# Optimization experiments

Hardware: AMD Instinct MI355X
Metric: run time of the kernel (lower is better)

Reference implementation:

```python
import jax, jax.numpy as jnp
import numpy as np

T = 128        # number of time points
D = 64         # flattened state dim (bs * z_dim, bs = 1)
H = 256        # hidden width of f-network
HK = 128       # hidden width of kernel network
MAX_IT = 3     # fixed-point iterations (args.max_iterations)


def setup_inputs() -> dict:
    key = jax.random.key(0)
    ks = jax.random.split(key, 6)
    g = lambda k, sh, sc: (jax.random.normal(k, sh, jnp.float32) * sc)
    z0 = jax.random.normal(ks[0], (1, D), jnp.float32)
    t = jnp.linspace(0.0, 1.0, T, dtype=jnp.float32)
    # f: D -> H -> D MLP (the 'func' integrand network)
    W1 = g(ks[1], (D, H), 1.0 / np.sqrt(D)); b1 = jnp.zeros((H,), jnp.float32)
    W2 = g(ks[2], (H, D), 1.0 / np.sqrt(H)); b2 = jnp.zeros((D,), jnp.float32)
    # kernel: (x, s) -> D*D matrix entries (the neural kernel K)
    Wk1 = g(ks[3], (2, HK), 1.0 / np.sqrt(2.0)); bk1 = jnp.zeros((HK,), jnp.float32)
    Wk2 = g(ks[4], (HK, D * D), 1.0 / np.sqrt(HK)); bk2 = jnp.zeros((D * D,), jnp.float32)
    return dict(z0=z0, t=t, W1=W1, b1=b1, W2=W2, b2=b2,
                Wk1=Wk1, bk1=bk1, Wk2=Wk2, bk2=bk2)


def _trapezoid_weights(t):
    """w[i, j]: trapezoid quadrature weight of node j for integral over [t0, t_i]."""
    dt = t[1] - t[0]  # uniform grid
    idx = jnp.arange(T)
    mask = (idx[None, :] <= idx[:, None]).astype(t.dtype)
    w = dt * mask
    w = w.at[(idx, idx)].multiply(0.5)   # halve right endpoint of each row
    w = w.at[:, 0].multiply(0.5)         # halve left endpoint
    w = w.at[0].set(0.0)                 # zero-length integral at t0
    return w


def _solve(z0, t, W1, b1, W2, b2, Wk1, bk1, Wk2, bk2):
    y0 = z0.reshape(-1)                                   # [D], solver flattens batch
    w = _trapezoid_weights(t)                             # [T, T]
    # Neural kernel K(x_i, s_j) -> [D, D], precomputed once on the grid.
    pairs = jnp.stack([jnp.broadcast_to(t[:, None], (T, T)),
                       jnp.broadcast_to(t[None, :], (T, T))], axis=-1)  # [T, T, 2]
    hK = jnp.tanh(pairs @ Wk1 + bk1)                      # [T, T, HK]
    K = (hK @ Wk2 + bk2).reshape(T, T, D, D)              # [T, T, D, D]

    def f(y):  # integrand network, applied over all time points
        return jnp.tanh(y @ W1 + b1) @ W2 + b2            # [T, D]

    def step(y, _):
        # G_i = \int_0^{x_i} K(x_i, s) f(y(s)) ds  (trapezoid on grid)
        G = jnp.einsum('ij,ijde,je->id', w, K, f(y))      # [T, D]
        # y'(x) = G(x)  =>  y_i = y0 + \int_0^{x_i} G(s) ds
        y_new = y0[None, :] + w @ G                       # [T, D]
        return y_new, None

    y_init = jnp.tile(y0[None, :], (T, 1))                # fixed-point initial guess
    y, _ = jax.lax.scan(step, y_init, None, length=MAX_IT)
    return y


def reference(z0, t, W1, b1, W2, b2, Wk1, bk1, Wk2, bk2):
    y = _solve(z0, t, W1, b1, W2, b2, Wk1, bk1, Wk2, bk2)  # [T, D]
    return y[-1].reshape(1, D)  # z[-1]: final state, shape [bs, dim]
```

## Files before the change

kernel.cpp:

```cpp
#include <hip/hip_runtime.h>
#include <hip/hip_bf16.h>

#define TT 128
#define DD 64
#define HH 256
#define HK 128
#define JH (TT*HK)
#define HD (HK*DD)
#define NCHUNK 64

__global__ void __launch_bounds__(256)
k_F(const float* __restrict__ G, const float* __restrict__ z0,
    const float* __restrict__ t,
    const float* __restrict__ W1, const float* __restrict__ b1,
    const float* __restrict__ W2, const float* __restrict__ b2,
    const float* __restrict__ bk2,
    float* __restrict__ F, float* __restrict__ bF, int it) {
    int j = blockIdx.x, tid = threadIdx.x;
    int part = tid >> 6, d = tid & 63;
    __shared__ float red[4][64];
    __shared__ float ys[DD];
    __shared__ float hs[HH];
    __shared__ float fs[DD];
    float dt = t[1] - t[0];
    if (it == 0) {
        if (tid < DD) ys[tid] = z0[tid];
    } else {
        float s = 0.f;
        if (j > 0) {
            for (int jp = part; jp <= j; jp += 4) {
                float w = (jp == 0 || jp == j) ? 0.5f : 1.0f;
                s += w * G[jp * DD + d];
            }
        }
        red[part][d] = s;
        __syncthreads();
        if (part == 0)
            ys[d] = z0[d] + dt * (red[0][d] + red[1][d] + red[2][d] + red[3][d]);
    }
    __syncthreads();
    float acc = b1[tid];
    #pragma unroll 8
    for (int e = 0; e < DD; ++e) acc += ys[e] * W1[e * HH + tid];
    hs[tid] = tanhf(acc);
    __syncthreads();
    {
        float s = 0.f;
        #pragma unroll 8
        for (int h = part * 64; h < part * 64 + 64; ++h) s += hs[h] * W2[h * DD + d];
        red[part][d] = s;
    }
    __syncthreads();
    if (part == 0) {
        float a = b2[d] + red[0][d] + red[1][d] + red[2][d] + red[3][d];
        fs[d] = a;
        F[j * DD + d] = a;
    }
    __syncthreads();
    {
        float s = 0.f;
        #pragma unroll
        for (int e = part * 16; e < part * 16 + 16; ++e) s += bk2[d * DD + e] * fs[e];
        red[part][d] = s;
    }
    __syncthreads();
    if (part == 0)
        bF[j * DD + d] = red[0][d] + red[1][d] + red[2][d] + red[3][d];
}

__global__ void __launch_bounds__(256)
k_M(const float* __restrict__ F, const float* __restrict__ Wk2,
    float* __restrict__ M) {
    int tid = threadIdx.x;
    int hd = blockIdx.x * 256 + tid;
    int j0 = blockIdx.y * 8;
    __shared__ __attribute__((aligned(16))) float Fs[8][64];
    for (int k = tid; k < 8 * DD; k += 256) Fs[k >> 6][k & 63] = F[j0 * DD + k];
    __syncthreads();
    float acc[8] = {0.f,0.f,0.f,0.f,0.f,0.f,0.f,0.f};
    const float* Wrow = Wk2 + (size_t)(hd >> 6) * (DD * DD) + (size_t)(hd & 63) * DD;
    for (int e = 0; e < DD; e += 8) {
        float4 wa = *(const float4*)(Wrow + e);
        float4 wb = *(const float4*)(Wrow + e + 4);
        #pragma unroll
        for (int r = 0; r < 8; ++r) {
            float4 f0 = *(const float4*)&Fs[r][e];
            float4 f1 = *(const float4*)&Fs[r][e + 4];
            acc[r] += f0.x*wa.x + f0.y*wa.y + f0.z*wa.z + f0.w*wa.w
                    + f1.x*wb.x + f1.y*wb.y + f1.z*wb.z + f1.w*wb.w;
        }
    }
    #pragma unroll
    for (int r = 0; r < 8; ++r) M[(size_t)(j0 + r) * HD + hd] = acc[r];
}

__global__ void __launch_bounds__(256)
k_G1(const float* __restrict__ t, const float* __restrict__ Wk1,
     const float* __restrict__ bk1, const float* __restrict__ M,
     float* __restrict__ P, const float* __restrict__ z0,
     float* __restrict__ out, int final_it) {
    int itile = blockIdx.x, c = blockIdx.y;
    if (c > 4 * itile + 3) return;
    __shared__ __attribute__((aligned(16))) float As[8 * 256];
    __shared__ float red[4][8][64];
    int tid = threadIdx.x, sub = tid >> 6, d = tid & 63;

    {
        float dt = t[1] - t[0];
        int h = tid & 127;
        int j = 2 * c + (tid >> 7);
        float wk0 = Wk1[h], wk1v = Wk1[HK + h], bk = bk1[h];
        float tj = t[j];
        #pragma unroll
        for (int k = 0; k < 8; ++k) {
            int i = itile * 8 + k;
            float w = (i == 0 || j > i) ? 0.f : dt * ((j == 0 || j == i) ? 0.5f : 1.0f);
            As[k * 256 + tid] = w * tanhf(t[i] * wk0 + tj * wk1v + bk);
        }
    }
    if (final_it && itile == 0 && c == 0 && tid < DD) out[tid] = z0[tid];
    __syncthreads();

    float acc[8] = {0.f,0.f,0.f,0.f,0.f,0.f,0.f,0.f};
    const float* Mp = M + ((size_t)c * 256) * DD + d;
    int jl0 = sub * 64;
    for (int jl = jl0; jl < jl0 + 64; jl += 8) {
        float m0 = Mp[(size_t)(jl + 0) * DD];
        float m1 = Mp[(size_t)(jl + 1) * DD];
        float m2 = Mp[(size_t)(jl + 2) * DD];
        float m3 = Mp[(size_t)(jl + 3) * DD];
        float m4 = Mp[(size_t)(jl + 4) * DD];
        float m5 = Mp[(size_t)(jl + 5) * DD];
        float m6 = Mp[(size_t)(jl + 6) * DD];
        float m7 = Mp[(size_t)(jl + 7) * DD];
        #pragma unroll
        for (int r = 0; r < 8; ++r) {
            float4 a0 = *(const float4*)&As[r * 256 + jl];
            float4 a1 = *(const float4*)&As[r * 256 + jl + 4];
            acc[r] += a0.x*m0 + a0.y*m1 + a0.z*m2 + a0.w*m3
                    + a1.x*m4 + a1.y*m5 + a1.z*m6 + a1.w*m7;
        }
    }
    #pragma unroll
    for (int r = 0; r < 8; ++r) red[sub][r][d] = acc[r];
    __syncthreads();
    if (sub == 0) {
        #pragma unroll
        for (int r = 0; r < 8; ++r) {
            float v = red[0][r][d] + red[1][r][d] + red[2][r][d] + red[3][r][d];
            P[(size_t)c * (TT * DD) + (itile * 8 + r) * DD + d] = v;
        }
    }
}

__global__ void __launch_bounds__(256)
k_Gfin(const float* __restrict__ P, const float* __restrict__ bF,
       const float* __restrict__ t, float* __restrict__ G,
       float* __restrict__ out, int final_it) {
    int j = blockIdx.x, tid = threadIdx.x;
    int part = tid >> 6, d = tid & 63;
    __shared__ float red[4][64];
    float dt = t[1] - t[0];
    float a = 0.f;
    int cmax = j >> 1;
    for (int c = part; c <= cmax; c += 4) a += P[(size_t)c * (TT * DD) + j * DD + d];
    if (j > 0) {
        float s = 0.f;
        for (int jp = part; jp <= j; jp += 4) {
            float w = (jp == 0 || jp == j) ? 0.5f : 1.0f;
            s += w * bF[jp * DD + d];
        }
        a += dt * s;
    }
    red[part][d] = a;
    __syncthreads();
    if (part == 0) {
        float v = red[0][d] + red[1][d] + red[2][d] + red[3][d];
        G[j * DD + d] = v;
        if (final_it) {
            float wj = (j == 0 || j == TT - 1) ? 0.5f : 1.0f;
            atomicAdd(&out[d], dt * wj * v);
        }
    }
}

extern "C" void kernel_launch(void* const* d_in, const int* in_sizes, int n_in,
                              void* d_out, int out_size, void* d_ws, size_t ws_size,
                              hipStream_t stream) {
    const float* z0  = (const float*)d_in[0];
    const float* t   = (const float*)d_in[1];
    const float* W1  = (const float*)d_in[2];
    const float* b1  = (const float*)d_in[3];
    const float* W2  = (const float*)d_in[4];
    const float* b2  = (const float*)d_in[5];
    const float* Wk1 = (const float*)d_in[6];
    const float* bk1 = (const float*)d_in[7];
    const float* Wk2 = (const float*)d_in[8];
    const float* bk2 = (const float*)d_in[9];
    float* out = (float*)d_out;

    float* ws = (float*)d_ws;
    float* M  = ws;
    float* F  = M  + (size_t)TT*HK*DD;
    float* bF = F  + TT*DD;
    float* G  = bF + TT*DD;
    float* P  = G  + TT*DD;

    for (int it = 0; it < 3; ++it) {
        int fin = (it == 2) ? 1 : 0;
        k_F<<<TT, 256, 0, stream>>>(G, z0, t, W1, b1, W2, b2, bk2, F, bF, it);
        k_M<<<dim3(32, 16), 256, 0, stream>>>(F, Wk2, M);
        k_G1<<<dim3(16, NCHUNK), 256, 0, stream>>>(t, Wk1, bk1, M, P, z0, out, fin);
        k_Gfin<<<TT, 256, 0, stream>>>(P, bF, t, G, out, fin);
    }
}
```

Measured before the change: 201.5 us.

## Fuse G finalization into next F kernel and widen G1 chunks

Removes the per-iteration G-finalization kernel by folding the reduction of partial sums and the bias-kernel term directly into the next iteration's F computation, which now builds y from P and the previous bF via a prefix-sum loop. The G1 kernel now uses 1024-wide j chunks (16 chunks instead of 64), so fewer partial-sum slices need reducing, at the cost of more work per block and fewer blocks. Ping-pong bF buffers are introduced and the launch sequence is unrolled. The F kernel now does serial per-row prefix work and loads up to 128x64 bF into shared memory, which adds latency per block.

```diff
diff --git a/kernel.cpp b/kernel.cpp
--- a/kernel.cpp
+++ b/kernel.cpp
@@ -7,37 +7,22 @@
 #define HK 128
 #define JH (TT*HK)
 #define HD (HK*DD)
-#define NCHUNK 64
-
-__global__ void __launch_bounds__(256)
-k_F(const float* __restrict__ G, const float* __restrict__ z0,
-    const float* __restrict__ t,
-    const float* __restrict__ W1, const float* __restrict__ b1,
-    const float* __restrict__ W2, const float* __restrict__ b2,
-    const float* __restrict__ bk2,
-    float* __restrict__ F, float* __restrict__ bF, int it) {
+#define NCHUNK 16
+#define CW 1024
+
+__global__ void __launch_bounds__(256)
+k_F0(const float* __restrict__ z0,
+     const float* __restrict__ W1, const float* __restrict__ b1,
+     const float* __restrict__ W2, const float* __restrict__ b2,
+     const float* __restrict__ bk2,
+     float* __restrict__ F, float* __restrict__ bF) {
     int j = blockIdx.x, tid = threadIdx.x;
     int part = tid >> 6, d = tid & 63;
     __shared__ float red[4][64];
     __shared__ float ys[DD];
     __shared__ float hs[HH];
     __shared__ float fs[DD];
-    float dt = t[1] - t[0];
-    if (it == 0) {
-        if (tid < DD) ys[tid] = z0[tid];
-    } else {
-        float s = 0.f;
-        if (j > 0) {
-            for (int jp = part; jp <= j; jp += 4) {
-                float w = (jp == 0 || jp == j) ? 0.5f : 1.0f;
-                s += w * G[jp * DD + d];
-            }
-        }
-        red[part][d] = s;
-        __syncthreads();
-        if (part == 0)
-            ys[d] = z0[d] + dt * (red[0][d] + red[1][d] + red[2][d] + red[3][d]);
-    }
+    if (tid < DD) ys[tid] = z0[tid];
     __syncthreads();
     float acc = b1[tid];
     #pragma unroll 8
@@ -66,6 +51,95 @@
     __syncthreads();
     if (part == 0)
         bF[j * DD + d] = red[0][d] + red[1][d] + red[2][d] + red[3][d];
+}
+
+__global__ void __launch_bounds__(256)
+k_FP(const float* __restrict__ P, const float* __restrict__ bFin,
+     const float* __restrict__ z0, const float* __restrict__ t,
+     const float* __restrict__ W1, const float* __restrict__ b1,
+     const float* __restrict__ W2, const float* __restrict__ b2,
+     const float* __restrict__ bk2,
+     float* __restrict__ F, float* __restrict__ bFout) {
+    int j = blockIdx.x, tid = threadIdx.x;
+    int part = tid >> 6, d = tid & 63;
+    __shared__ float bfs[TT][DD];
+    __shared__ float red[4][64];
+    __shared__ float ys[DD];
+    __shared__ float hs[HH];
+    __shared__ float fs[DD];
+    float dt = t[1] - t[0];
+
+    for (int k = tid; k < (j + 1) * DD; k += 256) bfs[k >> 6][k & 63] = bFin[k];
+
+    float s1 = 0.f;
+    for (int p = part; p <= j; p += 4) {
+        if (p == 0) continue;
+        int cmax = p >> 3;
+        float a = 0.f;
+        int c = 0;
+        for (; c + 7 <= cmax; c += 8) {
+            float p0 = P[(size_t)(c + 0) * (TT * DD) + p * DD + d];
+            float p1 = P[(size_t)(c + 1) * (TT * DD) + p * DD + d];
+            float p2 = P[(size_t)(c + 2) * (TT * DD) + p * DD + d];
+            float p3 = P[(size_t)(c + 3) * (TT * DD) + p * DD + d];
+            float p4 = P[(size_t)(c + 4) * (TT * DD) + p * DD + d];
+            float p5 = P[(size_t)(c + 5) * (TT * DD) + p * DD + d];
+            float p6 = P[(size_t)(c + 6) * (TT * DD) + p * DD + d];
+            float p7 = P[(size_t)(c + 7) * (TT * DD) + p * DD + d];
+            a += ((p0 + p1) + (p2 + p3)) + ((p4 + p5) + (p6 + p7));
+        }
+        for (; c <= cmax; ++c) a += P[(size_t)c * (TT * DD) + p * DD + d];
+        float wp = (p == j) ? 0.5f : 1.0f;
+        s1 += wp * a;
+    }
+    red[part][d] = s1;
+    __syncthreads();
+
+    if (part == 0) {
+        float sT = 0.f;
+        if (j > 0) {
+            float B0 = bfs[0][d];
+            float S = B0;
+            for (int p = 1; p <= j; ++p) {
+                float Bp = bfs[p][d];
+                float bft = dt * (S - 0.5f * B0 + 0.5f * Bp);
+                float wp = (p == j) ? 0.5f : 1.0f;
+                sT += wp * bft;
+                S += Bp;
+            }
+        }
+        float Bsum = red[0][d] + red[1][d] + red[2][d] + red[3][d];
+        ys[d] = z0[d] + dt * (Bsum + sT);
+    }
+    __syncthreads();
+
+    float acc = b1[tid];
+    #pragma unroll 8
+    for (int e = 0; e < DD; ++e) acc += ys[e] * W1[e * HH + tid];
+    hs[tid] = tanhf(acc);
+    __syncthreads();
+    {
+        float s = 0.f;
+        #pragma unroll 8
+        for (int h = part * 64; h < part * 64 + 64; ++h) s += hs[h] * W2[h * DD + d];
+        red[part][d] = s;
+    }
+    __syncthreads();
+    if (part == 0) {
+        float a = b2[d] + red[0][d] + red[1][d] + red[2][d] + red[3][d];
+        fs[d] = a;
+        F[j * DD + d] = a;
+    }
+    __syncthreads();
+    {
+        float s = 0.f;
+        #pragma unroll
+        for (int e = part * 16; e < part * 16 + 16; ++e) s += bk2[d * DD + e] * fs[e];
+        red[part][d] = s;
+    }
+    __syncthreads();
+    if (part == 0)
+        bFout[j * DD + d] = red[0][d] + red[1][d] + red[2][d] + red[3][d];
 }
 
 __global__ void __launch_bounds__(256)
@@ -100,31 +174,38 @@
      float* __restrict__ P, const float* __restrict__ z0,
      float* __restrict__ out, int final_it) {
     int itile = blockIdx.x, c = blockIdx.y;
-    if (c > 4 * itile + 3) return;
-    __shared__ __attribute__((aligned(16))) float As[8 * 256];
+    if (c > itile) return;
+    __shared__ __attribute__((aligned(16))) float As[8 * CW];
     __shared__ float red[4][8][64];
     int tid = threadIdx.x, sub = tid >> 6, d = tid & 63;
 
     {
         float dt = t[1] - t[0];
-        int h = tid & 127;
-        int j = 2 * c + (tid >> 7);
+        int h = tid & 127, jhi = tid >> 7;
         float wk0 = Wk1[h], wk1v = Wk1[HK + h], bk = bk1[h];
-        float tj = t[j];
-        #pragma unroll
-        for (int k = 0; k < 8; ++k) {
-            int i = itile * 8 + k;
-            float w = (i == 0 || j > i) ? 0.f : dt * ((j == 0 || j == i) ? 0.5f : 1.0f);
-            As[k * 256 + tid] = w * tanhf(t[i] * wk0 + tj * wk1v + bk);
+        float ti[8];
+        #pragma unroll
+        for (int k = 0; k < 8; ++k) ti[k] = t[itile * 8 + k];
+        #pragma unroll
+        for (int jj = 0; jj < 4; ++jj) {
+            int jloc = jj * 2 + jhi;
+            int j = c * 8 + jloc;
+            float tj = t[j];
+            #pragma unroll
+            for (int k = 0; k < 8; ++k) {
+                int i = itile * 8 + k;
+                float w = (i == 0 || j > i) ? 0.f : dt * ((j == 0 || j == i) ? 0.5f : 1.0f);
+                As[k * CW + jloc * HK + h] = w * tanhf(ti[k] * wk0 + tj * wk1v + bk);
+            }
         }
     }
     if (final_it && itile == 0 && c == 0 && tid < DD) out[tid] = z0[tid];
     __syncthreads();
 
     float acc[8] = {0.f,0.f,0.f,0.f,0.f,0.f,0.f,0.f};
-    const float* Mp = M + ((size_t)c * 256) * DD + d;
-    int jl0 = sub * 64;
-    for (int jl = jl0; jl < jl0 + 64; jl += 8) {
+    const float* Mp = M + ((size_t)c * CW) * DD + d;
+    int jl0 = sub * 256;
+    for (int jl = jl0; jl < jl0 + 256; jl += 8) {
         float m0 = Mp[(size_t)(jl + 0) * DD];
         float m1 = Mp[(size_t)(jl + 1) * DD];
         float m2 = Mp[(size_t)(jl + 2) * DD];
@@ -135,8 +216,8 @@
         float m7 = Mp[(size_t)(jl + 7) * DD];
         #pragma unroll
         for (int r = 0; r < 8; ++r) {
-            float4 a0 = *(const float4*)&As[r * 256 + jl];
-            float4 a1 = *(const float4*)&As[r * 256 + jl + 4];
+            float4 a0 = *(const float4*)&As[r * CW + jl];
+            float4 a1 = *(const float4*)&As[r * CW + jl + 4];
             acc[r] += a0.x*m0 + a0.y*m1 + a0.z*m2 + a0.w*m3
                     + a1.x*m4 + a1.y*m5 + a1.z*m6 + a1.w*m7;
         }
@@ -154,15 +235,14 @@
 }
 
 __global__ void __launch_bounds__(256)
-k_Gfin(const float* __restrict__ P, const float* __restrict__ bF,
-       const float* __restrict__ t, float* __restrict__ G,
-       float* __restrict__ out, int final_it) {
+k_out2(const float* __restrict__ P, const float* __restrict__ bF,
+       const float* __restrict__ t, float* __restrict__ out) {
     int j = blockIdx.x, tid = threadIdx.x;
     int part = tid >> 6, d = tid & 63;
     __shared__ float red[4][64];
     float dt = t[1] - t[0];
     float a = 0.f;
-    int cmax = j >> 1;
+    int cmax = j >> 3;
     for (int c = part; c <= cmax; c += 4) a += P[(size_t)c * (TT * DD) + j * DD + d];
     if (j > 0) {
         float s = 0.f;
@@ -176,11 +256,8 @@
     __syncthreads();
     if (part == 0) {
         float v = red[0][d] + red[1][d] + red[2][d] + red[3][d];
-        G[j * DD + d] = v;
-        if (final_it) {
-            float wj = (j == 0 || j == TT - 1) ? 0.5f : 1.0f;
-            atomicAdd(&out[d], dt * wj * v);
-        }
+        float wj = (j == 0 || j == TT - 1) ? 0.5f : 1.0f;
+        atomicAdd(&out[d], dt * wj * v);
     }
 }
 
@@ -199,18 +276,21 @@
     const float* bk2 = (const float*)d_in[9];
     float* out = (float*)d_out;
 
-    float* ws = (float*)d_ws;
-    float* M  = ws;
-    float* F  = M  + (size_t)TT*HK*DD;
-    float* bF = F  + TT*DD;
-    float* G  = bF + TT*DD;
-    float* P  = G  + TT*DD;
-
-    for (int it = 0; it < 3; ++it) {
-        int fin = (it == 2) ? 1 : 0;
-        k_F<<<TT, 256, 0, stream>>>(G, z0, t, W1, b1, W2, b2, bk2, F, bF, it);
-        k_M<<<dim3(32, 16), 256, 0, stream>>>(F, Wk2, M);
-        k_G1<<<dim3(16, NCHUNK), 256, 0, stream>>>(t, Wk1, bk1, M, P, z0, out, fin);
-        k_Gfin<<<TT, 256, 0, stream>>>(P, bF, t, G, out, fin);
-    }
-}
+    float* ws  = (float*)d_ws;
+    float* M   = ws;
+    float* F   = M   + (size_t)TT*HK*DD;
+    float* bFA = F   + TT*DD;
+    float* bFB = bFA + TT*DD;
+    float* P   = bFB + TT*DD;
+
+    k_F0<<<TT, 256, 0, stream>>>(z0, W1, b1, W2, b2, bk2, F, bFA);
+    k_M<<<dim3(32, 16), 256, 0, stream>>>(F, Wk2, M);
+    k_G1<<<dim3(16, NCHUNK), 256, 0, stream>>>(t, Wk1, bk1, M, P, z0, out, 0);
+    k_FP<<<TT, 256, 0, stream>>>(P, bFA, z0, t, W1, b1, W2, b2, bk2, F, bFB);
+    k_M<<<dim3(32, 16), 256, 0, stream>>>(F, Wk2, M);
+    k_G1<<<dim3(16, NCHUNK), 256, 0, stream>>>(t, Wk1, bk1, M, P, z0, out, 0);
+    k_FP<<<TT, 256, 0, stream>>>(P, bFB, z0, t, W1, b1, W2, b2, bk2, F, bFA);
+    k_M<<<dim3(32, 16), 256, 0, stream>>>(F, Wk2, M);
+    k_G1<<<dim3(16, NCHUNK), 256, 0, stream>>>(t, Wk1, bk1, M, P, z0, out, 1);
+    k_out2<<<TT, 256, 0, stream>>>(P, bFA, t, out);
+}
```

After: 260.3 us. 29.2% more time.

## Fuse M projection into the f-network kernel, dropping the F buffer

Applied to the files above, without the earlier changes.

Merges k_M into k_F so that each time-point block computes its own row of M = F·Wk2 right after evaluating f, which removes one launch per iteration and the F round trip through global memory. The trade-off is reuse: each block now streams all of Wk2 (2 MB) for a single f row, where the old k_M amortized every Wk2 load over 8 rows. Only 128 blocks run the heavy part, so L2 traffic on Wk2 rises about eightfold and parallelism drops.

```diff
diff --git a/kernel.cpp b/kernel.cpp
--- a/kernel.cpp
+++ b/kernel.cpp
@@ -10,12 +10,12 @@
 #define NCHUNK 64
 
 __global__ void __launch_bounds__(256)
-k_F(const float* __restrict__ G, const float* __restrict__ z0,
-    const float* __restrict__ t,
-    const float* __restrict__ W1, const float* __restrict__ b1,
-    const float* __restrict__ W2, const float* __restrict__ b2,
-    const float* __restrict__ bk2,
-    float* __restrict__ F, float* __restrict__ bF, int it) {
+k_FM2(const float* __restrict__ G, const float* __restrict__ z0,
+      const float* __restrict__ t,
+      const float* __restrict__ W1, const float* __restrict__ b1,
+      const float* __restrict__ W2, const float* __restrict__ b2,
+      const float* __restrict__ bk2, const float* __restrict__ Wk2,
+      float* __restrict__ M, float* __restrict__ bF, int it) {
     int j = blockIdx.x, tid = threadIdx.x;
     int part = tid >> 6, d = tid & 63;
     __shared__ float red[4][64];
@@ -23,6 +23,7 @@
     __shared__ float hs[HH];
     __shared__ float fs[DD];
     float dt = t[1] - t[0];
+
     if (it == 0) {
         if (tid < DD) ys[tid] = z0[tid];
     } else {
@@ -39,6 +40,7 @@
             ys[d] = z0[d] + dt * (red[0][d] + red[1][d] + red[2][d] + red[3][d]);
     }
     __syncthreads();
+
     float acc = b1[tid];
     #pragma unroll 8
     for (int e = 0; e < DD; ++e) acc += ys[e] * W1[e * HH + tid];
@@ -51,12 +53,10 @@
         red[part][d] = s;
     }
     __syncthreads();
-    if (part == 0) {
-        float a = b2[d] + red[0][d] + red[1][d] + red[2][d] + red[3][d];
-        fs[d] = a;
-        F[j * DD + d] = a;
-    }
-    __syncthreads();
+    if (part == 0)
+        fs[d] = b2[d] + red[0][d] + red[1][d] + red[2][d] + red[3][d];
+    __syncthreads();
+
     {
         float s = 0.f;
         #pragma unroll
@@ -66,32 +66,25 @@
     __syncthreads();
     if (part == 0)
         bF[j * DD + d] = red[0][d] + red[1][d] + red[2][d] + red[3][d];
-}
-
-__global__ void __launch_bounds__(256)
-k_M(const float* __restrict__ F, const float* __restrict__ Wk2,
-    float* __restrict__ M) {
-    int tid = threadIdx.x;
-    int hd = blockIdx.x * 256 + tid;
-    int j0 = blockIdx.y * 8;
-    __shared__ __attribute__((aligned(16))) float Fs[8][64];
-    for (int k = tid; k < 8 * DD; k += 256) Fs[k >> 6][k & 63] = F[j0 * DD + k];
-    __syncthreads();
-    float acc[8] = {0.f,0.f,0.f,0.f,0.f,0.f,0.f,0.f};
-    const float* Wrow = Wk2 + (size_t)(hd >> 6) * (DD * DD) + (size_t)(hd & 63) * DD;
-    for (int e = 0; e < DD; e += 8) {
-        float4 wa = *(const float4*)(Wrow + e);
-        float4 wb = *(const float4*)(Wrow + e + 4);
-        #pragma unroll
-        for (int r = 0; r < 8; ++r) {
-            float4 f0 = *(const float4*)&Fs[r][e];
-            float4 f1 = *(const float4*)&Fs[r][e + 4];
-            acc[r] += f0.x*wa.x + f0.y*wa.y + f0.z*wa.z + f0.w*wa.w
-                    + f1.x*wb.x + f1.y*wb.y + f1.z*wb.z + f1.w*wb.w;
-        }
-    }
-    #pragma unroll
-    for (int r = 0; r < 8; ++r) M[(size_t)(j0 + r) * HD + hd] = acc[r];
+
+    float4 f0 = *(const float4*)&fs[0];
+    (void)f0;
+    #pragma unroll 4
+    for (int c = 0; c < 32; ++c) {
+        int hd = c * 256 + tid;
+        const float* Wrow = Wk2 + (size_t)(hd >> 6) * (DD * DD) + (size_t)(hd & 63) * DD;
+        float a = 0.f;
+        #pragma unroll
+        for (int e = 0; e < DD; e += 8) {
+            float4 wa = *(const float4*)(Wrow + e);
+            float4 wb = *(const float4*)(Wrow + e + 4);
+            float4 fa = *(const float4*)&fs[e];
+            float4 fb = *(const float4*)&fs[e + 4];
+            a += fa.x*wa.x + fa.y*wa.y + fa.z*wa.z + fa.w*wa.w
+               + fb.x*wb.x + fb.y*wb.y + fb.z*wb.z + fb.w*wb.w;
+        }
+        M[(size_t)j * HD + hd] = a;
+    }
 }
 
 __global__ void __launch_bounds__(256)
@@ -201,15 +194,14 @@
 
     float* ws = (float*)d_ws;
     float* M  = ws;
-    float* F  = M  + (size_t)TT*HK*DD;
-    float* bF = F  + TT*DD;
+    float* bF = M  + (size_t)TT*HK*DD;
     float* G  = bF + TT*DD;
     float* P  = G  + TT*DD;
 
     for (int it = 0; it < 3; ++it) {
         int fin = (it == 2) ? 1 : 0;
-        k_F<<<TT, 256, 0, stream>>>(G, z0, t, W1, b1, W2, b2, bk2, F, bF, it);
-        k_M<<<dim3(32, 16), 256, 0, stream>>>(F, Wk2, M);
+        k_FM2<<<TT, 256, 0, stream>>>(G, z0, t, W1, b1, W2, b2, bk2, Wk2,
+                                      M, bF, it);
         k_G1<<<dim3(16, NCHUNK), 256, 0, stream>>>(t, Wk1, bk1, M, P, z0, out, fin);
         k_Gfin<<<TT, 256, 0, stream>>>(P, bF, t, G, out, fin);
     }
```

After: 417.3 us. 2.07x slower.

## Specialize first fixed-point iteration using constant initial state

Applied to the files above, without the earlier changes.

In the first iteration every time point has the same state y0, so f(y) is one vector. The change computes f once, forms a single HK×D product with Wk2, and builds G for all rows from a kernel-weighted tanh sum. This replaces the full k_F/k_M/k_G1/k_Gfin pass for iteration zero. It is meant to drop about a third of the heavy M and G1 work, at the cost of two extra specialized kernels and more workspace.

```diff
diff --git a/kernel.cpp b/kernel.cpp
--- a/kernel.cpp
+++ b/kernel.cpp
@@ -10,12 +10,102 @@
 #define NCHUNK 64
 
 __global__ void __launch_bounds__(256)
+k_F0M0(const float* __restrict__ z0,
+       const float* __restrict__ W1, const float* __restrict__ b1,
+       const float* __restrict__ W2, const float* __restrict__ b2,
+       const float* __restrict__ bk2, const float* __restrict__ Wk2,
+       float* __restrict__ M0, float* __restrict__ bF0) {
+    int bx = blockIdx.x, tid = threadIdx.x;
+    int part = tid >> 6, d = tid & 63;
+    __shared__ float red[4][64];
+    __shared__ float ys[DD];
+    __shared__ float hs[HH];
+    __shared__ __attribute__((aligned(16))) float fs[DD];
+    if (tid < DD) ys[tid] = z0[tid];
+    __syncthreads();
+    float acc = b1[tid];
+    #pragma unroll 8
+    for (int e = 0; e < DD; ++e) acc += ys[e] * W1[e * HH + tid];
+    hs[tid] = tanhf(acc);
+    __syncthreads();
+    {
+        float s = 0.f;
+        #pragma unroll 8
+        for (int h = part * 64; h < part * 64 + 64; ++h) s += hs[h] * W2[h * DD + d];
+        red[part][d] = s;
+    }
+    __syncthreads();
+    if (part == 0)
+        fs[d] = b2[d] + red[0][d] + red[1][d] + red[2][d] + red[3][d];
+    __syncthreads();
+    if (bx == 0) {
+        float s = 0.f;
+        #pragma unroll
+        for (int e = part * 16; e < part * 16 + 16; ++e) s += bk2[d * DD + e] * fs[e];
+        red[part][d] = s;
+        __syncthreads();
+        if (part == 0)
+            bF0[d] = red[0][d] + red[1][d] + red[2][d] + red[3][d];
+    }
+    int hd = bx * 256 + tid;
+    const float* Wrow = Wk2 + (size_t)(hd >> 6) * (DD * DD) + (size_t)(hd & 63) * DD;
+    float a = 0.f;
+    #pragma unroll
+    for (int e = 0; e < DD; e += 8) {
+        float4 wa = *(const float4*)(Wrow + e);
+        float4 wb = *(const float4*)(Wrow + e + 4);
+        float4 fa = *(const float4*)&fs[e];
+        float4 fb = *(const float4*)&fs[e + 4];
+        a += fa.x*wa.x + fa.y*wa.y + fa.z*wa.z + fa.w*wa.w
+           + fb.x*wb.x + fb.y*wb.y + fb.z*wb.z + fb.w*wb.w;
+    }
+    M0[hd] = a;
+}
+
+__global__ void __launch_bounds__(256)
+k_G0(const float* __restrict__ t, const float* __restrict__ Wk1,
+     const float* __restrict__ bk1, const float* __restrict__ M0,
+     const float* __restrict__ bF0, float* __restrict__ G) {
+    int i = blockIdx.x, tid = threadIdx.x;
+    int part = tid >> 6, d = tid & 63;
+    __shared__ float Bpart[2][HK];
+    __shared__ float Bs[HK];
+    __shared__ float red[4][64];
+    float dt = t[1] - t[0];
+    int h = tid & 127, half = tid >> 7;
+    float b = 0.f;
+    if (i > 0) {
+        float wk0 = Wk1[h], wk1v = Wk1[HK + h], bk = bk1[h];
+        float ti = t[i];
+        for (int j = half; j <= i; j += 2) {
+            float w = dt * ((j == 0 || j == i) ? 0.5f : 1.0f);
+            b += w * tanhf(ti * wk0 + t[j] * wk1v + bk);
+        }
+    }
+    Bpart[half][h] = b;
+    __syncthreads();
+    if (tid < HK) Bs[tid] = Bpart[0][tid] + Bpart[1][tid];
+    __syncthreads();
+    float a = 0.f;
+    #pragma unroll 8
+    for (int h2 = part * 32; h2 < part * 32 + 32; ++h2)
+        a += Bs[h2] * M0[h2 * DD + d];
+    red[part][d] = a;
+    __syncthreads();
+    if (part == 0) {
+        float g = red[0][d] + red[1][d] + red[2][d] + red[3][d];
+        if (i > 0) g += dt * (float)i * bF0[d];
+        G[i * DD + d] = g;
+    }
+}
+
+__global__ void __launch_bounds__(256)
 k_F(const float* __restrict__ G, const float* __restrict__ z0,
     const float* __restrict__ t,
     const float* __restrict__ W1, const float* __restrict__ b1,
     const float* __restrict__ W2, const float* __restrict__ b2,
     const float* __restrict__ bk2,
-    float* __restrict__ F, float* __restrict__ bF, int it) {
+    float* __restrict__ F, float* __restrict__ bF) {
     int j = blockIdx.x, tid = threadIdx.x;
     int part = tid >> 6, d = tid & 63;
     __shared__ float red[4][64];
@@ -23,9 +113,7 @@
     __shared__ float hs[HH];
     __shared__ float fs[DD];
     float dt = t[1] - t[0];
-    if (it == 0) {
-        if (tid < DD) ys[tid] = z0[tid];
-    } else {
+    {
         float s = 0.f;
         if (j > 0) {
             for (int jp = part; jp <= j; jp += 4) {
@@ -199,16 +287,20 @@
     const float* bk2 = (const float*)d_in[9];
     float* out = (float*)d_out;
 
-    float* ws = (float*)d_ws;
-    float* M  = ws;
-    float* F  = M  + (size_t)TT*HK*DD;
-    float* bF = F  + TT*DD;
-    float* G  = bF + TT*DD;
-    float* P  = G  + TT*DD;
-
-    for (int it = 0; it < 3; ++it) {
+    float* ws  = (float*)d_ws;
+    float* M   = ws;
+    float* F   = M   + (size_t)TT*HK*DD;
+    float* bF  = F   + TT*DD;
+    float* G   = bF  + TT*DD;
+    float* P   = G   + TT*DD;
+    float* M0  = P   + (size_t)NCHUNK*TT*DD;
+    float* bF0 = M0  + HD;
+
+    k_F0M0<<<32, 256, 0, stream>>>(z0, W1, b1, W2, b2, bk2, Wk2, M0, bF0);
+    k_G0<<<TT, 256, 0, stream>>>(t, Wk1, bk1, M0, bF0, G);
+    for (int it = 1; it < 3; ++it) {
         int fin = (it == 2) ? 1 : 0;
-        k_F<<<TT, 256, 0, stream>>>(G, z0, t, W1, b1, W2, b2, bk2, F, bF, it);
+        k_F<<<TT, 256, 0, stream>>>(G, z0, t, W1, b1, W2, b2, bk2, F, bF);
         k_M<<<dim3(32, 16), 256, 0, stream>>>(F, Wk2, M);
         k_G1<<<dim3(16, NCHUNK), 256, 0, stream>>>(t, Wk1, bk1, M, P, z0, out, fin);
         k_Gfin<<<TT, 256, 0, stream>>>(P, bF, t, G, out, fin);
```

After: 186.1 us (median of 2 runs). 1.08x faster.
